# Kernel optimization log

Measured on AMD Instinct MI355X. Metric: run time of the kernel, lower is better.

Reference implementation:

```python
import jax, jax.numpy as jnp
import numpy as np

LN_EPS = 1e-5


def setup_inputs() -> dict:
    key = jax.random.key(0)
    ks = jax.random.split(key, 12)
    B, S, D = 4, 1024, 1024
    s = 0.02
    return {
        "q": jax.random.normal(ks[0], (B, S, D), jnp.float32),
        "k": jax.random.normal(ks[1], (B, S, D), jnp.float32),
        "v": jax.random.normal(ks[2], (B, S, D), jnp.float32),
        "Wq": jax.random.normal(ks[3], (D, D), jnp.float32) * s,
        "bq": jnp.zeros((D,), jnp.float32),
        "Wk": jax.random.normal(ks[4], (D, D), jnp.float32) * s,
        "bk": jnp.zeros((D,), jnp.float32),
        "Wv": jax.random.normal(ks[5], (D, D), jnp.float32) * s,
        "bv": jnp.zeros((D,), jnp.float32),
        "Wo": jax.random.normal(ks[6], (D, D), jnp.float32) * s,
        "bo": jnp.zeros((D,), jnp.float32),
        "gamma": jnp.ones((D,), jnp.float32),
        "beta": jnp.zeros((D,), jnp.float32),
    }


def _mha(q, k, v, Wq, bq, Wk, bk, Wv, bv, Wo, bo, gamma, beta, h=16):
    B, Sq, D = q.shape
    Sk = k.shape[1]
    dv = D // h
    scale = dv ** 0.5
    # projections -> (B, h, S, dv)
    def proj(x, W, b, S):
        return (x @ W.T + b).reshape(B, S, h, dv).transpose(0, 2, 1, 3)
    Q = proj(q, Wq, bq, Sq)
    K = proj(k, Wk, bk, Sk)
    V = proj(v, Wv, bv, Sk)
    scores = jnp.einsum('bhqd,bhkd->bhqk', Q / scale, K)
    att = jax.nn.softmax(scores, axis=-1)  # (B,h,Sq,Sk)
    ctx = jnp.einsum('bhqk,bhkd->bhqd', att, V)
    ctx = ctx.transpose(0, 2, 1, 3).reshape(B, Sq, D)
    out = ctx @ Wo.T + bo
    x = q + out  # residual
    mu = jnp.mean(x, axis=-1, keepdims=True)
    var = jnp.mean(jnp.square(x - mu), axis=-1, keepdims=True)
    y = (x - mu) / jnp.sqrt(var + LN_EPS) * gamma + beta
    # att_score returned flattened over (B*h) as in the torch module
    return y, att.reshape(B * h, Sq, Sk)


def reference(q, k, v, Wq, bq, Wk, bk, Wv, bv, Wo, bo, gamma, beta):
    return _mha(q, k, v, Wq, bq, Wk, bk, Wv, bv, Wo, bo, gamma, beta)
```

## Files before the change

### kernel.cpp

```cpp
#include <hip/hip_runtime.h>
#include <stdint.h>

typedef __attribute__((ext_vector_type(4))) float f32x4;
typedef __attribute__((ext_vector_type(8))) short s16x8;
typedef __attribute__((ext_vector_type(8))) unsigned short u16x8;

#define MFMA16(a, b, c) __builtin_amdgcn_mfma_f32_16x16x32_bf16((a), (b), (c), 0, 0, 0)

__device__ __forceinline__ unsigned short f2bf(float f) {
  unsigned int u = __float_as_uint(f);
  u += 0x7fffu + ((u >> 16) & 1u);
  return (unsigned short)(u >> 16);
}

__device__ __forceinline__ void gll16(const unsigned short* g, unsigned short* l) {
  __builtin_amdgcn_global_load_lds((__attribute__((address_space(1))) void*)g,
                                   (__attribute__((address_space(3))) void*)l, 16, 0, 0);
}

__global__ __launch_bounds__(256) void cvt_kernel(
    const float* __restrict__ q, const float* __restrict__ k, const float* __restrict__ v,
    const float* __restrict__ Wq, const float* __restrict__ Wk,
    const float* __restrict__ Wv, const float* __restrict__ Wo,
    unsigned short* __restrict__ dst) {
  const size_t i = ((size_t)blockIdx.x * 256 + threadIdx.x) * 8;
  const size_t M1 = 4194304, W1 = 1048576;
  const float* src;
  if (i < M1) src = q + i;
  else if (i < 2 * M1) src = k + (i - M1);
  else if (i < 3 * M1) src = v + (i - 2 * M1);
  else {
    const size_t j = i - 3 * M1;
    src = (j < W1) ? Wq + j : (j < 2 * W1) ? Wk + (j - W1)
        : (j < 3 * W1) ? Wv + (j - 2 * W1) : Wo + (j - 3 * W1);
  }
  f32x4 a = *(const f32x4*)src;
  f32x4 c2 = *(const f32x4*)(src + 4);
  u16x8 o;
  o[0] = f2bf(a[0]);  o[1] = f2bf(a[1]);  o[2] = f2bf(a[2]);  o[3] = f2bf(a[3]);
  o[4] = f2bf(c2[0]); o[5] = f2bf(c2[1]); o[6] = f2bf(c2[2]); o[7] = f2bf(c2[3]);
  *(u16x8*)(dst + i) = o;
}

#define GEMM_PROLOG()                                                          \
  __shared__ unsigned short As[4096], Bs[4096];                                \
  const int lane = threadIdx.x & 63, wid = threadIdx.x >> 6;                   \
  const int g = lane >> 4, ln = lane & 15;                                     \
  const int wr = wid >> 1, wc = wid & 1;                                       \
  const int mt = blockIdx.y, nt = blockIdx.x;                                  \
  f32x4 acc[4][4];                                                             \
  { f32x4 z = {0.f, 0.f, 0.f, 0.f};                                            \
    _Pragma("unroll") for (int a_ = 0; a_ < 4; ++a_)                           \
      _Pragma("unroll") for (int b_ = 0; b_ < 4; ++b_) acc[a_][b_] = z; }      \
  const int c0 = wid * 64 + lane;                                              \
  const int row0 = c0 >> 2, cg0 = (c0 & 3) ^ ((row0 >> 1) & 3);                \
  const int c1 = 256 + c0;                                                     \
  const int row1 = c1 >> 2, cg1 = (c1 & 3) ^ ((row1 >> 1) & 3);

#define GEMM_KLOOP(Ag, Bg)                                                     \
  for (int kb = 0; kb < 32; ++kb) {                                            \
    gll16(Ag + (size_t)(mt * 128 + row0) * 1024 + kb * 32 + cg0 * 8,           \
          As + (size_t)(wid * 64) * 8);                                        \
    gll16(Bg + (size_t)(nt * 128 + row0) * 1024 + kb * 32 + cg0 * 8,           \
          Bs + (size_t)(wid * 64) * 8);                                        \
    gll16(Ag + (size_t)(mt * 128 + row1) * 1024 + kb * 32 + cg1 * 8,           \
          As + (size_t)(256 + wid * 64) * 8);                                  \
    gll16(Bg + (size_t)(nt * 128 + row1) * 1024 + kb * 32 + cg1 * 8,           \
          Bs + (size_t)(256 + wid * 64) * 8);                                  \
    __syncthreads();                                                           \
    s16x8 af[4], bf[4];                                                        \
    _Pragma("unroll") for (int mf = 0; mf < 4; ++mf) {                         \
      int rr = wr * 64 + mf * 16 + ln;                                         \
      af[mf] = *(const s16x8*)(As + rr * 32 + (g ^ ((rr >> 1) & 3)) * 8);      \
    }                                                                          \
    _Pragma("unroll") for (int nf = 0; nf < 4; ++nf) {                         \
      int rr = wc * 64 + nf * 16 + ln;                                         \
      bf[nf] = *(const s16x8*)(Bs + rr * 32 + (g ^ ((rr >> 1) & 3)) * 8);      \
    }                                                                          \
    _Pragma("unroll") for (int mf = 0; mf < 4; ++mf)                           \
      _Pragma("unroll") for (int nf = 0; nf < 4; ++nf)                         \
        acc[mf][nf] = MFMA16(af[mf], bf[nf], acc[mf][nf]);                     \
    __syncthreads();                                                           \
  }

__global__ __launch_bounds__(256) void gemm_qkv_kernel(
    const unsigned short* __restrict__ qb, const unsigned short* __restrict__ kb16,
    const unsigned short* __restrict__ vb,
    const unsigned short* __restrict__ Wqb, const unsigned short* __restrict__ Wkb,
    const unsigned short* __restrict__ Wvb,
    const float* __restrict__ bq, const float* __restrict__ bk, const float* __restrict__ bv,
    unsigned short* __restrict__ Qo, unsigned short* __restrict__ Ko,
    unsigned short* __restrict__ Vto) {
  const int z = blockIdx.z;
  const unsigned short* Ag = (z == 0) ? qb : (z == 1) ? kb16 : vb;
  const unsigned short* Bg = (z == 0) ? Wqb : (z == 1) ? Wkb : Wvb;
  const float* bias = (z == 0) ? bq : (z == 1) ? bk : bv;
  GEMM_PROLOG();
  GEMM_KLOOP(Ag, Bg);
  if (z < 2) {
    unsigned short* out = (z == 0) ? Qo : Ko;
#pragma unroll
    for (int nf = 0; nf < 4; ++nf) {
      const int col = nt * 128 + wc * 64 + nf * 16 + ln;
      const float bb = bias[col];
#pragma unroll
      for (int mf = 0; mf < 4; ++mf) {
        const int rowb = mt * 128 + wr * 64 + mf * 16 + g * 4;
#pragma unroll
        for (int r = 0; r < 4; ++r)
          out[(size_t)(rowb + r) * 1024 + col] = f2bf(acc[mf][nf][r] + bb);
      }
    }
  } else {
#pragma unroll
    for (int nf = 0; nf < 4; ++nf) {
      const int col = nt * 128 + wc * 64 + nf * 16 + ln;
      const float bb = bias[col];
      const int hh = col >> 6, d = col & 63;
#pragma unroll
      for (int mf = 0; mf < 4; ++mf) {
        const int rowb = mt * 128 + wr * 64 + mf * 16 + g * 4;
#pragma unroll
        for (int r = 0; r < 4; ++r) {
          const int row = rowb + r, b = row >> 10, s = row & 1023;
          Vto[(((size_t)b * 16 + hh) * 64 + d) * 1024 + s] = f2bf(acc[mf][nf][r] + bb);
        }
      }
    }
  }
}

__global__ __launch_bounds__(256) void gemm_o_kernel(
    const unsigned short* __restrict__ ctx, const unsigned short* __restrict__ Wob,
    const float* __restrict__ bo, const float* __restrict__ qres,
    float* __restrict__ x) {
  GEMM_PROLOG();
  GEMM_KLOOP(ctx, Wob);
#pragma unroll
  for (int nf = 0; nf < 4; ++nf) {
    const int col = nt * 128 + wc * 64 + nf * 16 + ln;
    const float bb = bo[col];
#pragma unroll
    for (int mf = 0; mf < 4; ++mf) {
      const int rowb = mt * 128 + wr * 64 + mf * 16 + g * 4;
#pragma unroll
      for (int r = 0; r < 4; ++r) {
        const size_t idx = (size_t)(rowb + r) * 1024 + col;
        x[idx] = acc[mf][nf][r] + bb + qres[idx];
      }
    }
  }
}

__global__ __launch_bounds__(512) void attn_kernel(
    const unsigned short* __restrict__ Q, const unsigned short* __restrict__ K,
    const unsigned short* __restrict__ Vt, unsigned short* __restrict__ ctx,
    float* __restrict__ att) {
  __shared__ unsigned short att_lds[32 * 1024];
  float* red = (float*)att_lds;

  const int tid = threadIdx.x;
  const int lane = tid & 63, wid = tid >> 6;
  const int g = lane >> 4, ln = lane & 15;
  const int wc = wid & 3, wr = wid >> 2;
  const int qb = blockIdx.x;
  const int bh = blockIdx.y;
  const int b = bh >> 4, h = bh & 15;
  const int s0 = qb * 32;
  const int arow = b * 1024 + s0;

  s16x8 aQ0, aQ1;
  {
    const unsigned short* qp = Q + (size_t)(arow + wr * 16 + ln) * 1024 + h * 64 + g * 8;
    aQ0 = *(const s16x8*)qp;
    aQ1 = *(const s16x8*)(qp + 32);
  }
  f32x4 sc[16];
  { f32x4 z = {0.f, 0.f, 0.f, 0.f};
#pragma unroll
    for (int nf = 0; nf < 16; ++nf) sc[nf] = z; }
  const unsigned short* kbase = K + (size_t)(b * 1024) * 1024 + h * 64 + g * 8;
#pragma unroll
  for (int nf = 0; nf < 16; ++nf) {
    const unsigned short* kp = kbase + (size_t)(wc * 256 + nf * 16 + ln) * 1024;
    s16x8 b0 = *(const s16x8*)kp;
    s16x8 b1 = *(const s16x8*)(kp + 32);
    sc[nf] = MFMA16(aQ0, b0, sc[nf]);
    sc[nf] = MFMA16(aQ1, b1, sc[nf]);
  }

  float m[4], rsum[4];
#pragma unroll
  for (int r = 0; r < 4; ++r) {
    float v = sc[0][r];
#pragma unroll
    for (int nf = 1; nf < 16; ++nf) v = fmaxf(v, sc[nf][r]);
#pragma unroll
    for (int off = 1; off < 16; off <<= 1) v = fmaxf(v, __shfl_xor(v, off));
    m[r] = v;
  }
  if (ln == 0) {
#pragma unroll
    for (int r = 0; r < 4; ++r) red[(wr * 4 + wc) * 16 + g * 4 + r] = m[r];
  }
  __syncthreads();
#pragma unroll
  for (int r = 0; r < 4; ++r) {
    float v = red[(wr * 4 + 0) * 16 + g * 4 + r];
    v = fmaxf(v, red[(wr * 4 + 1) * 16 + g * 4 + r]);
    v = fmaxf(v, red[(wr * 4 + 2) * 16 + g * 4 + r]);
    v = fmaxf(v, red[(wr * 4 + 3) * 16 + g * 4 + r]);
    m[r] = v;
  }
  const float cexp = 0.18033688011112042f;
#pragma unroll
  for (int r = 0; r < 4; ++r) rsum[r] = 0.f;
#pragma unroll
  for (int nf = 0; nf < 16; ++nf) {
#pragma unroll
    for (int r = 0; r < 4; ++r) {
      float p = __builtin_amdgcn_exp2f((sc[nf][r] - m[r]) * cexp);
      sc[nf][r] = p;
      rsum[r] += p;
    }
  }
#pragma unroll
  for (int r = 0; r < 4; ++r) {
    float v = rsum[r];
#pragma unroll
    for (int off = 1; off < 16; off <<= 1) v += __shfl_xor(v, off);
    rsum[r] = v;
  }
  if (ln == 0) {
#pragma unroll
    for (int r = 0; r < 4; ++r) red[128 + (wr * 4 + wc) * 16 + g * 4 + r] = rsum[r];
  }
  __syncthreads();
  float rinv[4];
#pragma unroll
  for (int r = 0; r < 4; ++r) {
    float v = red[128 + (wr * 4 + 0) * 16 + g * 4 + r] + red[128 + (wr * 4 + 1) * 16 + g * 4 + r] +
              red[128 + (wr * 4 + 2) * 16 + g * 4 + r] + red[128 + (wr * 4 + 3) * 16 + g * 4 + r];
    rinv[r] = __builtin_amdgcn_rcpf(v);
  }
  __syncthreads();

  float* aout = att + ((size_t)bh * 1024 + s0) * 1024;
#pragma unroll
  for (int nf = 0; nf < 16; ++nf) {
    const int colt = wc * 256 + nf * 16 + ln;
#pragma unroll
    for (int r = 0; r < 4; ++r) {
      const int rowt = wr * 16 + g * 4 + r;
      const float a = sc[nf][r] * rinv[r];
      aout[(size_t)rowt * 1024 + colt] = a;
      const int off = (rowt * 2048 + colt * 2) ^ ((rowt & 7) << 4);
      *(unsigned short*)((char*)att_lds + off) = f2bf(a);
    }
  }
  __syncthreads();

  f32x4 cacc = {0.f, 0.f, 0.f, 0.f};
  const unsigned short* vbase = Vt + ((size_t)bh * 64 + wc * 16 + ln) * 1024 + g * 8;
  const int row2 = wr * 16 + ln;
#pragma unroll 4
  for (int kk = 0; kk < 32; ++kk) {
    const int offa = (row2 * 2048 + kk * 64 + g * 16) ^ ((row2 & 7) << 4);
    s16x8 pa = *(const s16x8*)((const char*)att_lds + offa);
    s16x8 pb = *(const s16x8*)(vbase + kk * 32);
    cacc = MFMA16(pa, pb, cacc);
  }
  unsigned short* cp = ctx + (size_t)(arow + wr * 16 + g * 4) * 1024 + h * 64 + wc * 16 + ln;
#pragma unroll
  for (int r = 0; r < 4; ++r) cp[(size_t)r * 1024] = f2bf(cacc[r]);
}

__global__ __launch_bounds__(256) void ln_kernel(
    const float* __restrict__ x, const float* __restrict__ gamma,
    const float* __restrict__ beta, float* __restrict__ y) {
  const int row = blockIdx.x, t = threadIdx.x;
  const int lane = t & 63, wid = t >> 6;
  const float* xr = x + (size_t)row * 1024 + t * 4;
  f32x4 v = *(const f32x4*)xr;
  float s = v[0] + v[1] + v[2] + v[3];
#pragma unroll
  for (int off = 1; off < 64; off <<= 1) s += __shfl_xor(s, off);
  __shared__ float red1[4], red2[4];
  if (lane == 0) red1[wid] = s;
  __syncthreads();
  const float mu = (red1[0] + red1[1] + red1[2] + red1[3]) * (1.0f / 1024.0f);
  const float d0 = v[0] - mu, d1 = v[1] - mu, d2 = v[2] - mu, d3 = v[3] - mu;
  float ss = d0 * d0 + d1 * d1 + d2 * d2 + d3 * d3;
#pragma unroll
  for (int off = 1; off < 64; off <<= 1) ss += __shfl_xor(ss, off);
  if (lane == 0) red2[wid] = ss;
  __syncthreads();
  const float var = (red2[0] + red2[1] + red2[2] + red2[3]) * (1.0f / 1024.0f);
  const float rstd = rsqrtf(var + 1e-5f);
  f32x4 gv = *(const f32x4*)(gamma + t * 4);
  f32x4 bv = *(const f32x4*)(beta + t * 4);
  f32x4 o;
  o[0] = d0 * rstd * gv[0] + bv[0];
  o[1] = d1 * rstd * gv[1] + bv[1];
  o[2] = d2 * rstd * gv[2] + bv[2];
  o[3] = d3 * rstd * gv[3] + bv[3];
  *(f32x4*)(y + (size_t)row * 1024 + t * 4) = o;
}

extern "C" void kernel_launch(void* const* d_in, const int* in_sizes, int n_in,
                              void* d_out, int out_size, void* d_ws, size_t ws_size,
                              hipStream_t stream) {
  const float* q  = (const float*)d_in[0];
  const float* k  = (const float*)d_in[1];
  const float* v  = (const float*)d_in[2];
  const float* Wq = (const float*)d_in[3];
  const float* bq = (const float*)d_in[4];
  const float* Wk = (const float*)d_in[5];
  const float* bk = (const float*)d_in[6];
  const float* Wv = (const float*)d_in[7];
  const float* bv = (const float*)d_in[8];
  const float* Wo = (const float*)d_in[9];
  const float* bo = (const float*)d_in[10];
  const float* gamma = (const float*)d_in[11];
  const float* beta  = (const float*)d_in[12];

  char* ws = (char*)d_ws;
  unsigned short* conv = (unsigned short*)ws;
  unsigned short* qb16 = conv;
  unsigned short* kb16 = conv + 4194304;
  unsigned short* vb16 = conv + 2 * 4194304;
  unsigned short* Wqb  = conv + 3 * 4194304;
  unsigned short* Wkb  = Wqb + 1048576;
  unsigned short* Wvb  = Wkb + 1048576;
  unsigned short* Wob  = Wvb + 1048576;
  unsigned short* Qb  = (unsigned short*)(ws + (32u << 20));
  unsigned short* Kb  = (unsigned short*)(ws + (40u << 20));
  unsigned short* Vtb = (unsigned short*)(ws + (48u << 20));
  unsigned short* ctx = (unsigned short*)(ws + (56u << 20));
  float* x = (float*)(ws + (32u << 20));

  float* y_out = (float*)d_out;
  float* att_out = y_out + 4194304;

  cvt_kernel<<<8192, 256, 0, stream>>>(q, k, v, Wq, Wk, Wv, Wo, conv);
  dim3 gq(8, 32, 3);
  gemm_qkv_kernel<<<gq, 256, 0, stream>>>(qb16, kb16, vb16, Wqb, Wkb, Wvb,
                                          bq, bk, bv, Qb, Kb, Vtb);
  dim3 ga(32, 64, 1);
  attn_kernel<<<ga, 512, 0, stream>>>(Qb, Kb, Vtb, ctx, att_out);
  dim3 go(8, 32, 1);
  gemm_o_kernel<<<go, 256, 0, stream>>>(ctx, Wob, bo, q, x);
  ln_kernel<<<4096, 256, 0, stream>>>(x, gamma, beta, y_out);
}
```

Measured before the change: 537.6 us.

## Double-buffer GEMM LDS tiles and vectorize attention-score stores via LDS

The GEMM k-loop now uses two LDS buffers, issuing the global-to-LDS loads for the next k-step before computing the current one, with one barrier per iteration instead of two. This hides load latency at the cost of doubled LDS per block. In the attention kernel, the fp32 score output is no longer written as scattered scalar stores. It is re-read from the bf16 LDS tile and written as coalesced float4 stores, and the LDS swizzle gains an extra XOR term to avoid bank conflicts. The returned attention probabilities are therefore rounded to bf16 precision, which risks accuracy tolerance.

```diff
diff --git a/kernel.cpp b/kernel.cpp
--- a/kernel.cpp
+++ b/kernel.cpp
@@ -4,6 +4,7 @@
 typedef __attribute__((ext_vector_type(4))) float f32x4;
 typedef __attribute__((ext_vector_type(8))) short s16x8;
 typedef __attribute__((ext_vector_type(8))) unsigned short u16x8;
+typedef __attribute__((ext_vector_type(4))) unsigned short u16x4;
 
 #define MFMA16(a, b, c) __builtin_amdgcn_mfma_f32_16x16x32_bf16((a), (b), (c), 0, 0, 0)
 
@@ -43,7 +44,7 @@
 }
 
 #define GEMM_PROLOG()                                                          \
-  __shared__ unsigned short As[4096], Bs[4096];                                \
+  __shared__ unsigned short As[8192], Bs[8192];                                \
   const int lane = threadIdx.x & 63, wid = threadIdx.x >> 6;                   \
   const int g = lane >> 4, ln = lane & 15;                                     \
   const int wr = wid >> 1, wc = wid & 1;                                       \
@@ -57,31 +58,41 @@
   const int c1 = 256 + c0;                                                     \
   const int row1 = c1 >> 2, cg1 = (c1 & 3) ^ ((row1 >> 1) & 3);
 
-#define GEMM_KLOOP(Ag, Bg)                                                     \
-  for (int kb = 0; kb < 32; ++kb) {                                            \
-    gll16(Ag + (size_t)(mt * 128 + row0) * 1024 + kb * 32 + cg0 * 8,           \
-          As + (size_t)(wid * 64) * 8);                                        \
-    gll16(Bg + (size_t)(nt * 128 + row0) * 1024 + kb * 32 + cg0 * 8,           \
-          Bs + (size_t)(wid * 64) * 8);                                        \
-    gll16(Ag + (size_t)(mt * 128 + row1) * 1024 + kb * 32 + cg1 * 8,           \
-          As + (size_t)(256 + wid * 64) * 8);                                  \
-    gll16(Bg + (size_t)(nt * 128 + row1) * 1024 + kb * 32 + cg1 * 8,           \
-          Bs + (size_t)(256 + wid * 64) * 8);                                  \
-    __syncthreads();                                                           \
-    s16x8 af[4], bf[4];                                                        \
+#define GEMM_STAGE(Ag, Bg, kb, buf)                                            \
+    gll16(Ag + (size_t)(mt * 128 + row0) * 1024 + (kb) * 32 + cg0 * 8,         \
+          As + (buf) * 4096 + wid * 512);                                      \
+    gll16(Bg + (size_t)(nt * 128 + row0) * 1024 + (kb) * 32 + cg0 * 8,         \
+          Bs + (buf) * 4096 + wid * 512);                                      \
+    gll16(Ag + (size_t)(mt * 128 + row1) * 1024 + (kb) * 32 + cg1 * 8,         \
+          As + (buf) * 4096 + 2048 + wid * 512);                               \
+    gll16(Bg + (size_t)(nt * 128 + row1) * 1024 + (kb) * 32 + cg1 * 8,         \
+          Bs + (buf) * 4096 + 2048 + wid * 512);
+
+#define GEMM_COMPUTE(buf)                                                      \
+  { s16x8 af[4], bf[4];                                                        \
     _Pragma("unroll") for (int mf = 0; mf < 4; ++mf) {                         \
       int rr = wr * 64 + mf * 16 + ln;                                         \
-      af[mf] = *(const s16x8*)(As + rr * 32 + (g ^ ((rr >> 1) & 3)) * 8);      \
+      af[mf] = *(const s16x8*)(As + (buf) * 4096 + rr * 32 +                   \
+                               (g ^ ((rr >> 1) & 3)) * 8);                     \
     }                                                                          \
     _Pragma("unroll") for (int nf = 0; nf < 4; ++nf) {                         \
       int rr = wc * 64 + nf * 16 + ln;                                         \
-      bf[nf] = *(const s16x8*)(Bs + rr * 32 + (g ^ ((rr >> 1) & 3)) * 8);      \
+      bf[nf] = *(const s16x8*)(Bs + (buf) * 4096 + rr * 32 +                   \
+                               (g ^ ((rr >> 1) & 3)) * 8);                     \
     }                                                                          \
     _Pragma("unroll") for (int mf = 0; mf < 4; ++mf)                           \
       _Pragma("unroll") for (int nf = 0; nf < 4; ++nf)                         \
-        acc[mf][nf] = MFMA16(af[mf], bf[nf], acc[mf][nf]);                     \
+        acc[mf][nf] = MFMA16(af[mf], bf[nf], acc[mf][nf]); }
+
+#define GEMM_KLOOP(Ag, Bg)                                                     \
+  GEMM_STAGE(Ag, Bg, 0, 0)                                                     \
+  __syncthreads();                                                             \
+  for (int kb = 0; kb < 31; ++kb) {                                            \
+    GEMM_STAGE(Ag, Bg, kb + 1, (kb + 1) & 1)                                   \
+    GEMM_COMPUTE(kb & 1)                                                       \
     __syncthreads();                                                           \
-  }
+  }                                                                            \
+  GEMM_COMPUTE(1)
 
 __global__ __launch_bounds__(256) void gemm_qkv_kernel(
     const unsigned short* __restrict__ qb, const unsigned short* __restrict__ kb16,
@@ -245,27 +256,43 @@
   }
   __syncthreads();
 
-  float* aout = att + ((size_t)bh * 1024 + s0) * 1024;
 #pragma unroll
   for (int nf = 0; nf < 16; ++nf) {
     const int colt = wc * 256 + nf * 16 + ln;
+    const int cx = ((colt >> 6) & 7) << 4;
 #pragma unroll
     for (int r = 0; r < 4; ++r) {
       const int rowt = wr * 16 + g * 4 + r;
-      const float a = sc[nf][r] * rinv[r];
-      aout[(size_t)rowt * 1024 + colt] = a;
-      const int off = (rowt * 2048 + colt * 2) ^ ((rowt & 7) << 4);
-      *(unsigned short*)((char*)att_lds + off) = f2bf(a);
-    }
-  }
-  __syncthreads();
+      const int off = (rowt * 2048 + colt * 2) ^ ((rowt & 7) << 4) ^ cx;
+      *(unsigned short*)((char*)att_lds + off) = f2bf(sc[nf][r] * rinv[r]);
+    }
+  }
+  __syncthreads();
+
+  {
+    float* abase = att + ((size_t)bh * 1024 + s0) * 1024;
+#pragma unroll
+    for (int j = 0; j < 16; ++j) {
+      const int ci = j * 512 + tid;
+      const int row = ci >> 8;
+      const int col = (ci & 255) * 4;
+      const int off = (row * 2048 + col * 2) ^ ((row & 7) << 4) ^ (((col >> 6) & 7) << 4);
+      u16x4 pv = *(const u16x4*)((const char*)att_lds + off);
+      f32x4 o;
+      o[0] = __uint_as_float((unsigned)(unsigned short)pv[0] << 16);
+      o[1] = __uint_as_float((unsigned)(unsigned short)pv[1] << 16);
+      o[2] = __uint_as_float((unsigned)(unsigned short)pv[2] << 16);
+      o[3] = __uint_as_float((unsigned)(unsigned short)pv[3] << 16);
+      *(f32x4*)(abase + ci * 4) = o;
+    }
+  }
 
   f32x4 cacc = {0.f, 0.f, 0.f, 0.f};
   const unsigned short* vbase = Vt + ((size_t)bh * 64 + wc * 16 + ln) * 1024 + g * 8;
   const int row2 = wr * 16 + ln;
 #pragma unroll 4
   for (int kk = 0; kk < 32; ++kk) {
-    const int offa = (row2 * 2048 + kk * 64 + g * 16) ^ ((row2 & 7) << 4);
+    const int offa = (row2 * 2048 + kk * 64 + g * 16) ^ ((row2 & 7) << 4) ^ (((kk >> 1) & 7) << 4);
     s16x8 pa = *(const s16x8*)((const char*)att_lds + offa);
     s16x8 pb = *(const s16x8*)(vbase + kk * 32);
     cacc = MFMA16(pa, pb, cacc);
```

New measurement: 541.2 us. About the same (+0.7%).
